# Optimization experiments

Hardware: AMD Instinct MI355X
Metric: run time of the kernel (lower is better)

## Reference

```python
import jax, jax.numpy as jnp
import numpy as np

DIM = 128
B, NQ, NK = 4, 4096, 4096
SCALE = DIM ** -0.5


def setup_inputs() -> dict:
    key = jax.random.key(0)
    ks = jax.random.split(key, 13)
    def lin(k, shape, scale=0.02):
        return jax.random.normal(k, shape, dtype=jnp.float32) * scale
    return {
        "query": jax.random.normal(ks[0], (B, NQ, DIM), dtype=jnp.float32),
        "key": jax.random.normal(ks[1], (B, NK, DIM), dtype=jnp.float32),
        "value": jax.random.normal(ks[2], (B, NK, DIM), dtype=jnp.float32),
        "att_bias": jax.random.normal(ks[3], (B, NK), dtype=jnp.float32),
        # params, [in, out] layout (torch Linear is x @ W.T + b)
        "q_w": lin(ks[4], (DIM, DIM)), "q_b": jnp.zeros((DIM,), jnp.float32),
        "k_w": lin(ks[5], (DIM, DIM)),
        "v_w": lin(ks[6], (DIM, DIM)), "v_b": jnp.zeros((DIM,), jnp.float32),
        "vs_w": lin(ks[7], (DIM, 1)), "vs_b": jnp.zeros((1,), jnp.float32),
        "p_w": lin(ks[8], (DIM, DIM)), "p_b": jnp.zeros((DIM,), jnp.float32),
    }


def reference(query, key, value, att_bias, q_w, q_b, k_w, v_w, v_b, vs_w, vs_b, p_w, p_b):
    # projections
    q = query @ q_w + q_b                      # [B, NQ, D]
    k = key @ k_w                              # [B, NK, D] (no bias)
    v = value @ v_w + v_b                      # [B, NK, D]
    # per-key semantic scalar, broadcast over queries: [B, 1, NK]
    semantic = (value @ vs_w + vs_b).reshape(value.shape[0], 1, value.shape[1])
    # scores + biases
    attn = jnp.einsum('bqd,bkd->bqk', q, k) * SCALE + semantic
    attn = attn + att_bias[:, None, :]
    attn = jax.nn.softmax(attn, axis=-1)
    out = jnp.einsum('bqk,bkd->bqd', attn, v)  # [B, NQ, D]
    out = out @ p_w + p_b
    return out
```

## Files before the change

### kernel.cpp

```cpp
#include <hip/hip_runtime.h>

typedef __bf16 bf16x8 __attribute__((ext_vector_type(8)));
typedef float f32x4 __attribute__((ext_vector_type(4)));

#define MFMA16(a,b,c) __builtin_amdgcn_mfma_f32_16x16x32_bf16(a,b,c,0,0,0)

static __device__ __forceinline__ unsigned short f2bf(float f){
  union{float f;unsigned u;}v; v.f=f;
  unsigned u=v.u;
  u += 0x7fffu + ((u>>16)&1u);
  return (unsigned short)(u>>16);
}
static __device__ __forceinline__ float bf2f(unsigned short h){
  union{unsigned u;float f;}v; v.u=((unsigned)h)<<16; return v.f;
}
static __device__ __forceinline__ unsigned cvtpk(float lo, float hi){
  unsigned r;
  asm("v_cvt_pk_bf16_f32 %0, %1, %2" : "=v"(r) : "v"(lo), "v"(hi));
  return r;
}
static __device__ __forceinline__ void gload16(const void* g, void* l){
  __builtin_amdgcn_global_load_lds(
    (const __attribute__((address_space(1))) unsigned int*)(uintptr_t)g,
    (__attribute__((address_space(3))) unsigned int*)(uintptr_t)l,
    16, 0, 0);
}

#define SCALE_QK 0.08838834764831845f
#define LOG2E    1.44269504088896340f
#define THR_L2   11.541560327111708f

#define SWZ128(r,c) (((r)<<7) + ((c) ^ (((r)&7)<<3)))


__global__ __launch_bounds__(256) void k_proj(
    const float* __restrict__ query, const float* __restrict__ key,
    const float* __restrict__ value, const float* __restrict__ att_bias,
    const float* __restrict__ q_w, const float* __restrict__ q_b,
    const float* __restrict__ k_w, const float* __restrict__ v_w,
    const float* __restrict__ v_b, const float* __restrict__ vs_w,
    const float* __restrict__ vs_b,
    unsigned short* __restrict__ qp, unsigned short* __restrict__ kp,
    unsigned short* __restrict__ vpt, float* __restrict__ biasc)
{
  const int t = blockIdx.y;
  const float* X = (t==0) ? query : ((t==1) ? key : value);
  const float* W = (t==0) ? q_w  : ((t==1) ? k_w : v_w);
  const int tid = threadIdx.x;
  const int row0 = blockIdx.x * 64;

  __shared__ __align__(16) unsigned short Wt[128][136];
  __shared__ __align__(16) unsigned short Xs[64][136];
  __shared__ float vsw_s[128];

  #pragma unroll 4
  for (int i=0;i<16;i++){
    int idx = tid*64 + i*4;
    float4 v4 = *(const float4*)(W + idx);
    Wt[(idx+0)&127][(idx+0)>>7] = f2bf(v4.x);
    Wt[(idx+1)&127][(idx+1)>>7] = f2bf(v4.y);
    Wt[(idx+2)&127][(idx+2)>>7] = f2bf(v4.z);
    Wt[(idx+3)&127][(idx+3)>>7] = f2bf(v4.w);
  }
  {
    const float* Xb = X + (size_t)row0*128;
    #pragma unroll
    for (int i=0;i<8;i++){
      int f4 = i*256 + tid;
      int row = f4>>5, c4 = f4&31;
      float4 v = *(const float4*)(Xb + row*128 + c4*4);
      ushort4 h;
      h.x = f2bf(v.x); h.y = f2bf(v.y); h.z = f2bf(v.z); h.w = f2bf(v.w);
      *(ushort4*)&Xs[row][c4*4] = h;
    }
  }
  if (t==2 && tid<128) vsw_s[tid] = vs_w[tid];
  __syncthreads();

  const int w = tid>>6, lane = tid&63, lr = lane&15, lg = lane>>4;
  f32x4 acc[8];
  #pragma unroll
  for (int nt=0;nt<8;nt++) acc[nt] = (f32x4){0.f,0.f,0.f,0.f};
  #pragma unroll
  for (int kk=0;kk<4;kk++){
    bf16x8 a = *(const bf16x8*)&Xs[w*16+lr][kk*32+lg*8];
    #pragma unroll
    for (int nt=0;nt<8;nt++){
      bf16x8 bb = *(const bf16x8*)&Wt[nt*16+lr][kk*32+lg*8];
      acc[nt] = MFMA16(a,bb,acc[nt]);
    }
  }

  if (t < 2){
    const float* bias = (t==0) ? q_b : (const float*)nullptr;
    const float sc = (t==0) ? (SCALE_QK*LOG2E) : 1.f;
    unsigned short* dstm = (t==0) ? qp : kp;
    #pragma unroll
    for (int nt=0;nt<8;nt++){
      int col = nt*16+lr;
      float bv = bias ? bias[col] : 0.f;
      #pragma unroll
      for (int r=0;r<4;r++){
        int row = row0 + w*16 + lg*4 + r;
        dstm[(size_t)row*128+col] = f2bf((acc[nt][r] + bv) * sc);
      }
    }
  } else {
    {
      int rl = tid>>2, part = tid&3;
      float s = 0.f;
      #pragma unroll
      for (int j=0;j<32;j++){
        int d = part*32+j;
        s += bf2f(Xs[rl][d]) * vsw_s[d];
      }
      s += __shfl_xor(s,1);
      s += __shfl_xor(s,2);
      if ((tid&3)==0){
        int rg = row0 + rl;
        biasc[rg] = (s + vs_b[0] + att_bias[rg]) * LOG2E;
      }
    }
    __syncthreads();
    unsigned short* Vls = (unsigned short*)Wt;
    #pragma unroll
    for (int nt=0;nt<8;nt++){
      int col = nt*16+lr;
      float bv = v_b[col];
      #pragma unroll
      for (int r=0;r<4;r++){
        int rl_ = w*16 + lg*4 + r;
        int k5 = rl_ & 31;
        int pos = 8*((k5>>2)&3) + (k5&3) + 4*(k5>>4);
        int np = (rl_ & 32) | pos;
        Vls[col*72 + np] = f2bf(acc[nt][r] + bv);
      }
    }
    __syncthreads();
    int d = tid>>1, half = tid&1;
    int bi = row0>>12, n0 = row0&4095;
    unsigned short* dst = vpt + ((size_t)(bi*128+d))*4096 + n0 + half*32;
    const unsigned short* src = Vls + d*72 + half*32;
    #pragma unroll
    for (int i=0;i<4;i++)
      *(uint4*)(dst + i*8) = *(const uint4*)(src + i*8);
  }
}

__global__ __launch_bounds__(256,4) void k_flash(
    const unsigned short* __restrict__ qp, const unsigned short* __restrict__ kp,
    const unsigned short* __restrict__ vpt, const float* __restrict__ biasc,
    unsigned short* __restrict__ opart, float* __restrict__ ml)
{
  const int f = blockIdx.x;
  const int xcd = f & 7, slot = f >> 3;
  const int group = xcd*4 + (slot>>6);
  const int b = group>>3, split = group&7;
  const int q0 = (slot & 63) * 64;

  const int tid = threadIdx.x;
  const int w = tid>>6, lane = tid&63;
  const int q15 = lane&15, g = lane>>4;

  __shared__ __align__(16) unsigned short Ks[2][32*128];
  __shared__ __align__(16) unsigned short Vs[2][128*32];

  const unsigned short* kbase = kp  + (size_t)(b*4096 + split*512)*128;
  const unsigned short* vbase = vpt + (size_t)b*128*4096 + split*512;
  const float* bbase = biasc + b*4096 + split*512;

  bf16x8 qf[4];
  {
    const unsigned short* qrow = qp + ((size_t)(b*4096 + q0 + w*16 + q15))*128;
    #pragma unroll
    for (int kk=0;kk<4;kk++) qf[kk] = *(const bf16x8*)(qrow + kk*32 + g*8);
  }

  #define STAGE(bf_, k0_) do{                                                 \
    const char* kb_ = (const char*)kbase + (size_t)(k0_)*256;                 \
    const char* vb_ = (const char*)vbase + (size_t)(k0_)*2;                   \
    _Pragma("unroll")                                                         \
    for (int i=0;i<2;i++){                                                    \
      int s_ = w*2+i;                                                         \
      int kr = s_*4 + (lane>>4);                                              \
      gload16(kb_ + kr*256 + (((lane&15)*16) ^ ((kr&7)*16)),                  \
              (char*)Ks[bf_] + s_*1024);                                      \
      int vd = s_*16 + (lane>>2);                                             \
      gload16(vb_ + (size_t)vd*8192 + (((lane&3) ^ (vd&3))*16),               \
              (char*)Vs[bf_] + s_*1024);                                      \
    }                                                                         \
  }while(0)

  float m_run = -INFINITY, l_run = 0.f;
  f32x4 acc[8];
  #pragma unroll
  for (int nt=0;nt<8;nt++) acc[nt] = (f32x4){0.f,0.f,0.f,0.f};

  STAGE(0, 0);
  __syncthreads();

  const int voff = (q15<<6) + ((g ^ (q15&3))<<4);

  for (int t=0;t<16;t++){
    const int cur = t & 1;
    if (t<15) STAGE(cur^1, (t+1)*32);

    const float* Bt = bbase + t*32;
    float4 b0 = *(const float4*)(Bt + g*4);
    float4 b1 = *(const float4*)(Bt + 16 + g*4);

    const unsigned short* Kc = Ks[cur];
    const char* Vc = (const char*)Vs[cur];

    f32x4 s0 = {}, s1 = {};
    __builtin_amdgcn_s_setprio(1);
    #pragma unroll
    for (int kk=0;kk<4;kk++){
      bf16x8 a0 = *(const bf16x8*)&Kc[SWZ128(q15,      kk*32 + g*8)];
      bf16x8 a1 = *(const bf16x8*)&Kc[SWZ128(16 + q15, kk*32 + g*8)];
      s0 = MFMA16(a0, qf[kk], s0);
      s1 = MFMA16(a1, qf[kk], s1);
    }
    __builtin_amdgcn_s_setprio(0);

    float tmax = -1e30f;
    #pragma unroll
    for (int c=0;c<4;c++){
      s0[c] += ((const float*)&b0)[c];
      s1[c] += ((const float*)&b1)[c];
      tmax = fmaxf(tmax, fmaxf(s0[c], s1[c]));
    }
    tmax = fmaxf(tmax, __shfl_xor(tmax, 16));
    tmax = fmaxf(tmax, __shfl_xor(tmax, 32));

    if (!__all(tmax <= m_run + THR_L2)){
      float mn = fmaxf(m_run, tmax);
      float corr = __builtin_exp2f(m_run - mn);
      m_run = mn;
      l_run *= corr;
      float c0 = __shfl(corr, g*4+0);
      float c1 = __shfl(corr, g*4+1);
      float c2 = __shfl(corr, g*4+2);
      float c3 = __shfl(corr, g*4+3);
      #pragma unroll
      for (int nt=0;nt<8;nt++){
        acc[nt][0]*=c0; acc[nt][1]*=c1; acc[nt][2]*=c2; acc[nt][3]*=c3;
      }
    }

    float rs = 0.f;
    #pragma unroll
    for (int c=0;c<4;c++){
      s0[c] = __builtin_exp2f(s0[c]-m_run); rs += s0[c];
      s1[c] = __builtin_exp2f(s1[c]-m_run); rs += s1[c];
    }
    rs += __shfl_xor(rs, 16);
    rs += __shfl_xor(rs, 32);
    l_run += rs;

    union { unsigned u[4]; bf16x8 v; } pu;
    pu.u[0] = cvtpk(s0[0], s0[1]);
    pu.u[1] = cvtpk(s0[2], s0[3]);
    pu.u[2] = cvtpk(s1[0], s1[1]);
    pu.u[3] = cvtpk(s1[2], s1[3]);

    __builtin_amdgcn_s_setprio(1);
    #pragma unroll
    for (int nt=0;nt<8;nt++){
      bf16x8 vf = *(const bf16x8*)(Vc + voff + nt*1024);
      acc[nt] = MFMA16(pu.v, vf, acc[nt]);
    }
    __builtin_amdgcn_s_setprio(0);

    __syncthreads();
  }
  #undef STAGE

  const size_t rowbase = (size_t)split*16384 + (size_t)b*4096 + q0;
  float i0 = 1.f/__shfl(l_run, g*4+0);
  float i1 = 1.f/__shfl(l_run, g*4+1);
  float i2 = 1.f/__shfl(l_run, g*4+2);
  float i3 = 1.f/__shfl(l_run, g*4+3);
  #pragma unroll
  for (int nt=0;nt<8;nt++){
    int col = nt*16 + q15;
    size_t rb = rowbase + w*16 + g*4;
    opart[(rb+0)*128 + col] = f2bf(acc[nt][0]*i0);
    opart[(rb+1)*128 + col] = f2bf(acc[nt][1]*i1);
    opart[(rb+2)*128 + col] = f2bf(acc[nt][2]*i2);
    opart[(rb+3)*128 + col] = f2bf(acc[nt][3]*i3);
  }
  if (lane < 16){
    size_t rg = rowbase + w*16 + lane;
    ml[rg*2]   = m_run;
    ml[rg*2+1] = l_run;
  }
}

__global__ __launch_bounds__(256) void k_outproj(
    const unsigned short* __restrict__ opart, const float* __restrict__ ml,
    const float* __restrict__ p_w, const float* __restrict__ p_b,
    float* __restrict__ out)
{
  const int tid = threadIdx.x;
  const int row0 = blockIdx.x*32;
  __shared__ __align__(16) unsigned short Wt[128][136];
  __shared__ __align__(16) unsigned short Xs[32][136];
  __shared__ float wmg[8][32];

  #pragma unroll 4
  for (int i=0;i<16;i++){
    int idx = tid*64 + i*4;
    float4 v4 = *(const float4*)(p_w + idx);
    Wt[(idx+0)&127][(idx+0)>>7] = f2bf(v4.x);
    Wt[(idx+1)&127][(idx+1)>>7] = f2bf(v4.y);
    Wt[(idx+2)&127][(idx+2)>>7] = f2bf(v4.z);
    Wt[(idx+3)&127][(idx+3)>>7] = f2bf(v4.w);
  }
  if (tid < 32){
    int row = row0 + tid;
    float m[8], l[8];
    #pragma unroll
    for (int i=0;i<8;i++){
      m[i] = ml[((size_t)i*16384 + row)*2];
      l[i] = ml[((size_t)i*16384 + row)*2 + 1];
    }
    float M = m[0];
    #pragma unroll
    for (int i=1;i<8;i++) M = fmaxf(M, m[i]);
    float wi[8], wsum = 0.f;
    #pragma unroll
    for (int i=0;i<8;i++){ wi[i] = __builtin_exp2f(m[i]-M)*l[i]; wsum += wi[i]; }
    float inv = 1.f/wsum;
    #pragma unroll
    for (int i=0;i<8;i++) wmg[i][tid] = wi[i]*inv;
  }
  __syncthreads();
  #pragma unroll
  for (int i=0;i<2;i++){
    int e = (i*256 + tid)*8;
    int row = e>>7, col = e&127;
    float a8[8];
    #pragma unroll
    for (int j=0;j<8;j++) a8[j] = 0.f;
    #pragma unroll
    for (int s=0;s<8;s++){
      uint4 v = *(const uint4*)(opart + ((size_t)s*16384 + row0 + row)*128 + col);
      float wv = wmg[s][row];
      const unsigned short* hp = (const unsigned short*)&v;
      #pragma unroll
      for (int j=0;j<8;j++) a8[j] += wv * bf2f(hp[j]);
    }
    unsigned short h8[8];
    #pragma unroll
    for (int j=0;j<8;j++) h8[j] = f2bf(a8[j]);
    *(uint4*)&Xs[row][col] = *(const uint4*)h8;
  }
  __syncthreads();

  const int w=tid>>6, lane=tid&63, lr=lane&15, lg=lane>>4;
  const int r0 = (w&1)*16, c0 = (w>>1)*64;
  f32x4 acc[4];
  #pragma unroll
  for (int nt=0;nt<4;nt++) acc[nt] = (f32x4){0.f,0.f,0.f,0.f};
  #pragma unroll
  for (int kk=0;kk<4;kk++){
    bf16x8 a = *(const bf16x8*)&Xs[r0+lr][kk*32+lg*8];
    #pragma unroll
    for (int nt=0;nt<4;nt++){
      bf16x8 bb = *(const bf16x8*)&Wt[c0+nt*16+lr][kk*32+lg*8];
      acc[nt] = MFMA16(a,bb,acc[nt]);
    }
  }
  __syncthreads();
  float* Os = (float*)Wt;
  #pragma unroll
  for (int nt=0;nt<4;nt++){
    int col = c0 + nt*16 + lr;
    float pb = p_b[col];
    #pragma unroll
    for (int r=0;r<4;r++){
      int row = r0 + lg*4 + r;
      Os[row*132 + col] = acc[nt][r] + pb;
    }
  }
  __syncthreads();
  {
    int row = tid>>3, seg = tid&7;
    const float* src = Os + row*132 + seg*16;
    float* dst = out + (size_t)(row0+row)*128 + seg*16;
    #pragma unroll
    for (int i=0;i<4;i++)
      *(float4*)(dst + i*4) = *(const float4*)(src + i*4);
  }
}

extern "C" void kernel_launch(void* const* d_in, const int* in_sizes, int n_in,
                              void* d_out, int out_size, void* d_ws, size_t ws_size,
                              hipStream_t stream) {
  (void)in_sizes; (void)n_in; (void)out_size; (void)ws_size;
  const float* query    = (const float*)d_in[0];
  const float* key      = (const float*)d_in[1];
  const float* value    = (const float*)d_in[2];
  const float* att_bias = (const float*)d_in[3];
  const float* q_w = (const float*)d_in[4];
  const float* q_b = (const float*)d_in[5];
  const float* k_w = (const float*)d_in[6];
  const float* v_w = (const float*)d_in[7];
  const float* v_b = (const float*)d_in[8];
  const float* vs_w = (const float*)d_in[9];
  const float* vs_b = (const float*)d_in[10];
  const float* p_w = (const float*)d_in[11];
  const float* p_b = (const float*)d_in[12];

  char* ws = (char*)d_ws;
  unsigned short* qp    = (unsigned short*)(ws);
  unsigned short* kp    = (unsigned short*)(ws + 4194304);
  unsigned short* vpt   = (unsigned short*)(ws + 8388608);
  float*          biasc = (float*)(ws + 12582912);
  unsigned short* opart = (unsigned short*)(ws + 12648448);
  float*          ml    = (float*)(ws + 46202880);

  hipLaunchKernelGGL(k_proj, dim3(256,3), dim3(256), 0, stream,
    query,key,value,att_bias,q_w,q_b,k_w,v_w,v_b,vs_w,vs_b,qp,kp,vpt,biasc);
  hipLaunchKernelGGL(k_flash, dim3(2048), dim3(256), 0, stream,
    qp,kp,vpt,biasc,opart,ml);
  hipLaunchKernelGGL(k_outproj, dim3(512), dim3(256), 0, stream,
    opart,ml,p_w,p_b,(float*)d_out);
}
```

Measured before the change: 90.34 us.

## Switch flash kernel to 32x32x16 MFMA with 2 waves per block

The flash attention kernel moves from 16x16x32 to 32x32x16 bf16 MFMA tiles, so each wave handles 32 query rows and the block drops to 128 threads (2 waves) covering the same 64 queries. The V permutation written by the projection kernel and the LDS staging and swizzle for V are reworked to match the new operand layout, and bias loads are hoisted ahead of staging. The aim is fewer MFMA issues and fewer LDS fragment reads per score tile, plus fewer cross-lane shuffles for row max and sum. In exchange, accumulator register pressure rises and there are fewer waves per block for hiding latency.

```diff
diff --git a/kernel.cpp b/kernel.cpp
--- a/kernel.cpp
+++ b/kernel.cpp
@@ -2,8 +2,10 @@
 
 typedef __bf16 bf16x8 __attribute__((ext_vector_type(8)));
 typedef float f32x4 __attribute__((ext_vector_type(4)));
+typedef float f32x16 __attribute__((ext_vector_type(16)));
 
 #define MFMA16(a,b,c) __builtin_amdgcn_mfma_f32_16x16x32_bf16(a,b,c,0,0,0)
+#define MFMA32(a,b,c) __builtin_amdgcn_mfma_f32_32x32x16_bf16(a,b,c,0,0,0)
 
 static __device__ __forceinline__ unsigned short f2bf(float f){
   union{float f;unsigned u;}v; v.f=f;
@@ -131,7 +133,7 @@
       for (int r=0;r<4;r++){
         int rl_ = w*16 + lg*4 + r;
         int k5 = rl_ & 31;
-        int pos = 8*((k5>>2)&3) + (k5&3) + 4*(k5>>4);
+        int pos = 16*(k5>>4) + (k5&3) + 4*((k5>>3)&1) + 8*((k5>>2)&1);
         int np = (rl_ & 32) | pos;
         Vls[col*72 + np] = f2bf(acc[nt][r] + bv);
       }
@@ -147,7 +149,7 @@
   }
 }
 
-__global__ __launch_bounds__(256,4) void k_flash(
+__global__ __launch_bounds__(128,3) void k_flash(
     const unsigned short* __restrict__ qp, const unsigned short* __restrict__ kp,
     const unsigned short* __restrict__ vpt, const float* __restrict__ biasc,
     unsigned short* __restrict__ opart, float* __restrict__ ml)
@@ -160,77 +162,81 @@
 
   const int tid = threadIdx.x;
   const int w = tid>>6, lane = tid&63;
-  const int q15 = lane&15, g = lane>>4;
+  const int l31 = lane&31, hi = lane>>5;
 
   __shared__ __align__(16) unsigned short Ks[2][32*128];
-  __shared__ __align__(16) unsigned short Vs[2][128*32];
+  __shared__ __align__(16) char Vp[2][8192];
 
   const unsigned short* kbase = kp  + (size_t)(b*4096 + split*512)*128;
-  const unsigned short* vbase = vpt + (size_t)b*128*4096 + split*512;
+  const char* vbase = (const char*)(vpt + (size_t)b*128*4096 + split*512);
   const float* bbase = biasc + b*4096 + split*512;
 
-  bf16x8 qf[4];
+  bf16x8 qf[8];
   {
-    const unsigned short* qrow = qp + ((size_t)(b*4096 + q0 + w*16 + q15))*128;
-    #pragma unroll
-    for (int kk=0;kk<4;kk++) qf[kk] = *(const bf16x8*)(qrow + kk*32 + g*8);
+    const unsigned short* qrow = qp + ((size_t)(b*4096 + q0 + w*32 + l31))*128;
+    #pragma unroll
+    for (int kk=0;kk<8;kk++) qf[kk] = *(const bf16x8*)(qrow + kk*16 + hi*8);
   }
 
   #define STAGE(bf_, k0_) do{                                                 \
     const char* kb_ = (const char*)kbase + (size_t)(k0_)*256;                 \
-    const char* vb_ = (const char*)vbase + (size_t)(k0_)*2;                   \
+    const char* vb_ = vbase + (size_t)(k0_)*2;                                \
     _Pragma("unroll")                                                         \
-    for (int i=0;i<2;i++){                                                    \
-      int s_ = w*2+i;                                                         \
+    for (int i=0;i<4;i++){                                                    \
+      int s_ = w*4+i;                                                         \
       int kr = s_*4 + (lane>>4);                                              \
       gload16(kb_ + kr*256 + (((lane&15)*16) ^ ((kr&7)*16)),                  \
               (char*)Ks[bf_] + s_*1024);                                      \
-      int vd = s_*16 + (lane>>2);                                             \
-      gload16(vb_ + (size_t)vd*8192 + (((lane&3) ^ (vd&3))*16),               \
-              (char*)Vs[bf_] + s_*1024);                                      \
+      int u_ = (lane&7) ^ ((lane>>3)&7);                                      \
+      int vd = s_*16 + ((lane>>3)<<1) + (u_>>2);                              \
+      gload16(vb_ + (size_t)vd*8192 + ((u_&3)<<4),                            \
+              (char*)Vp[bf_] + s_*1024);                                      \
     }                                                                         \
   }while(0)
 
   float m_run = -INFINITY, l_run = 0.f;
-  f32x4 acc[8];
-  #pragma unroll
-  for (int nt=0;nt<8;nt++) acc[nt] = (f32x4){0.f,0.f,0.f,0.f};
+  f32x16 acc[4];
+  #pragma unroll
+  for (int dt=0;dt<4;dt++) acc[dt] = (f32x16){};
 
   STAGE(0, 0);
   __syncthreads();
 
-  const int voff = (q15<<6) + ((g ^ (q15&3))<<4);
+  const int vA = (l31>>1)*128;
+  const int vX = ((l31>>1)&7)<<4;
+  const int vH = (l31&1)*64 + hi*16;
 
   for (int t=0;t<16;t++){
     const int cur = t & 1;
+    const float* Bt = bbase + t*32 + hi*4;
+    float4 b0 = *(const float4*)(Bt);
+    float4 b1 = *(const float4*)(Bt + 8);
+    float4 b2 = *(const float4*)(Bt + 16);
+    float4 b3 = *(const float4*)(Bt + 24);
     if (t<15) STAGE(cur^1, (t+1)*32);
 
-    const float* Bt = bbase + t*32;
-    float4 b0 = *(const float4*)(Bt + g*4);
-    float4 b1 = *(const float4*)(Bt + 16 + g*4);
-
     const unsigned short* Kc = Ks[cur];
-    const char* Vc = (const char*)Vs[cur];
-
-    f32x4 s0 = {}, s1 = {};
+    const char* Vc = Vp[cur];
+
+    f32x16 sc = {};
     __builtin_amdgcn_s_setprio(1);
     #pragma unroll
-    for (int kk=0;kk<4;kk++){
-      bf16x8 a0 = *(const bf16x8*)&Kc[SWZ128(q15,      kk*32 + g*8)];
-      bf16x8 a1 = *(const bf16x8*)&Kc[SWZ128(16 + q15, kk*32 + g*8)];
-      s0 = MFMA16(a0, qf[kk], s0);
-      s1 = MFMA16(a1, qf[kk], s1);
+    for (int kk=0;kk<8;kk++){
+      bf16x8 a = *(const bf16x8*)&Kc[SWZ128(l31, kk*16 + hi*8)];
+      sc = MFMA32(a, qf[kk], sc);
     }
     __builtin_amdgcn_s_setprio(0);
 
     float tmax = -1e30f;
     #pragma unroll
     for (int c=0;c<4;c++){
-      s0[c] += ((const float*)&b0)[c];
-      s1[c] += ((const float*)&b1)[c];
-      tmax = fmaxf(tmax, fmaxf(s0[c], s1[c]));
-    }
-    tmax = fmaxf(tmax, __shfl_xor(tmax, 16));
+      sc[c]    += ((const float*)&b0)[c];
+      sc[4+c]  += ((const float*)&b1)[c];
+      sc[8+c]  += ((const float*)&b2)[c];
+      sc[12+c] += ((const float*)&b3)[c];
+    }
+    #pragma unroll
+    for (int i=0;i<16;i++) tmax = fmaxf(tmax, sc[i]);
     tmax = fmaxf(tmax, __shfl_xor(tmax, 32));
 
     if (!__all(tmax <= m_run + THR_L2)){
@@ -238,37 +244,39 @@
       float corr = __builtin_exp2f(m_run - mn);
       m_run = mn;
       l_run *= corr;
-      float c0 = __shfl(corr, g*4+0);
-      float c1 = __shfl(corr, g*4+1);
-      float c2 = __shfl(corr, g*4+2);
-      float c3 = __shfl(corr, g*4+3);
       #pragma unroll
-      for (int nt=0;nt<8;nt++){
-        acc[nt][0]*=c0; acc[nt][1]*=c1; acc[nt][2]*=c2; acc[nt][3]*=c3;
+      for (int r=0;r<16;r++){
+        int qn = (r&3) + 8*(r>>2) + 4*hi;
+        float ca = __shfl(corr, qn);
+        acc[0][r]*=ca; acc[1][r]*=ca; acc[2][r]*=ca; acc[3][r]*=ca;
       }
     }
 
     float rs = 0.f;
     #pragma unroll
-    for (int c=0;c<4;c++){
-      s0[c] = __builtin_exp2f(s0[c]-m_run); rs += s0[c];
-      s1[c] = __builtin_exp2f(s1[c]-m_run); rs += s1[c];
-    }
-    rs += __shfl_xor(rs, 16);
+    for (int i=0;i<16;i++){
+      sc[i] = __builtin_exp2f(sc[i]-m_run); rs += sc[i];
+    }
     rs += __shfl_xor(rs, 32);
     l_run += rs;
 
-    union { unsigned u[4]; bf16x8 v; } pu;
-    pu.u[0] = cvtpk(s0[0], s0[1]);
-    pu.u[1] = cvtpk(s0[2], s0[3]);
-    pu.u[2] = cvtpk(s1[0], s1[1]);
-    pu.u[3] = cvtpk(s1[2], s1[3]);
+    union { unsigned u[4]; bf16x8 v; } pu0, pu1;
+    pu0.u[0] = cvtpk(sc[0],  sc[1]);
+    pu0.u[1] = cvtpk(sc[2],  sc[3]);
+    pu0.u[2] = cvtpk(sc[4],  sc[5]);
+    pu0.u[3] = cvtpk(sc[6],  sc[7]);
+    pu1.u[0] = cvtpk(sc[8],  sc[9]);
+    pu1.u[1] = cvtpk(sc[10], sc[11]);
+    pu1.u[2] = cvtpk(sc[12], sc[13]);
+    pu1.u[3] = cvtpk(sc[14], sc[15]);
 
     __builtin_amdgcn_s_setprio(1);
     #pragma unroll
-    for (int nt=0;nt<8;nt++){
-      bf16x8 vf = *(const bf16x8*)(Vc + voff + nt*1024);
-      acc[nt] = MFMA16(pu.v, vf, acc[nt]);
+    for (int dt=0;dt<4;dt++){
+      bf16x8 v0 = *(const bf16x8*)(Vc + dt*2048 + vA + ((vH +  0) ^ vX));
+      bf16x8 v1 = *(const bf16x8*)(Vc + dt*2048 + vA + ((vH + 32) ^ vX));
+      acc[dt] = MFMA32(pu0.v, v0, acc[dt]);
+      acc[dt] = MFMA32(pu1.v, v1, acc[dt]);
     }
     __builtin_amdgcn_s_setprio(0);
 
@@ -277,21 +285,18 @@
   #undef STAGE
 
   const size_t rowbase = (size_t)split*16384 + (size_t)b*4096 + q0;
-  float i0 = 1.f/__shfl(l_run, g*4+0);
-  float i1 = 1.f/__shfl(l_run, g*4+1);
-  float i2 = 1.f/__shfl(l_run, g*4+2);
-  float i3 = 1.f/__shfl(l_run, g*4+3);
-  #pragma unroll
-  for (int nt=0;nt<8;nt++){
-    int col = nt*16 + q15;
-    size_t rb = rowbase + w*16 + g*4;
-    opart[(rb+0)*128 + col] = f2bf(acc[nt][0]*i0);
-    opart[(rb+1)*128 + col] = f2bf(acc[nt][1]*i1);
-    opart[(rb+2)*128 + col] = f2bf(acc[nt][2]*i2);
-    opart[(rb+3)*128 + col] = f2bf(acc[nt][3]*i3);
-  }
-  if (lane < 16){
-    size_t rg = rowbase + w*16 + lane;
+  #pragma unroll
+  for (int r=0;r<16;r++){
+    int qn = (r&3) + 8*(r>>2) + 4*hi;
+    float inv = 1.f/__shfl(l_run, qn);
+    size_t row = rowbase + w*32 + qn;
+    opart[row*128 +      l31] = f2bf(acc[0][r]*inv);
+    opart[row*128 + 32 + l31] = f2bf(acc[1][r]*inv);
+    opart[row*128 + 64 + l31] = f2bf(acc[2][r]*inv);
+    opart[row*128 + 96 + l31] = f2bf(acc[3][r]*inv);
+  }
+  if (hi==0){
+    size_t rg = rowbase + w*32 + l31;
     ml[rg*2]   = m_run;
     ml[rg*2+1] = l_run;
   }
@@ -423,7 +428,7 @@
 
   hipLaunchKernelGGL(k_proj, dim3(256,3), dim3(256), 0, stream,
     query,key,value,att_bias,q_w,q_b,k_w,v_w,v_b,vs_w,vs_b,qp,kp,vpt,biasc);
-  hipLaunchKernelGGL(k_flash, dim3(2048), dim3(256), 0, stream,
+  hipLaunchKernelGGL(k_flash, dim3(2048), dim3(128), 0, stream,
     qp,kp,vpt,biasc,opart,ml);
   hipLaunchKernelGGL(k_outproj, dim3(512), dim3(256), 0, stream,
     opart,ml,p_w,p_b,(float*)d_out);
```

Result: slower. 107.3 us (+18.7%).
